# Kernel optimization log

Measured on AMD Instinct MI355X. Metric: run time of the kernel, lower is better.

Reference implementation:

```python
import jax, jax.numpy as jnp
import numpy as np

POOL = 7
IMG_H, IMG_W = 1024, 1024
CANONICAL = 224.0  # canonical box size used in the FPN level assignment


def _crop_and_resize(fm, boxes, ph, pw):
    """TF-style crop_and_resize (extrapolation_value=0).

    fm: [C, H, W] feature map; boxes: [N, 4] normalized (y1, x1, y2, x2).
    Returns [N, C, ph, pw] bilinearly sampled crops.
    """
    C, H, W = fm.shape
    y1, x1, y2, x2 = boxes[:, 0], boxes[:, 1], boxes[:, 2], boxes[:, 3]
    ty = jnp.arange(ph, dtype=boxes.dtype) / (ph - 1)  # [ph] in [0,1]
    tx = jnp.arange(pw, dtype=boxes.dtype) / (pw - 1)
    ys = (y1[:, None] + (y2 - y1)[:, None] * ty) * (H - 1)  # [N, ph] image coords
    xs = (x1[:, None] + (x2 - x1)[:, None] * tx) * (W - 1)  # [N, pw]
    yy = jnp.broadcast_to(ys[:, :, None], (ys.shape[0], ph, pw))  # [N, ph, pw]
    xx = jnp.broadcast_to(xs[:, None, :], (xs.shape[0], ph, pw))
    y0f = jnp.floor(yy)
    x0f = jnp.floor(xx)
    wy = yy - y0f
    wx = xx - x0f
    y0 = jnp.clip(y0f.astype(jnp.int32), 0, H - 1)
    y1i = jnp.clip(y0 + 1, 0, H - 1)
    x0 = jnp.clip(x0f.astype(jnp.int32), 0, W - 1)
    x1i = jnp.clip(x0 + 1, 0, W - 1)

    def g(yi, xi):
        return fm[:, yi, xi]  # [C, N, ph, pw]

    val = (g(y0, x0) * ((1 - wy) * (1 - wx))[None]
           + g(y0, x1i) * ((1 - wy) * wx)[None]
           + g(y1i, x0) * (wy * (1 - wx))[None]
           + g(y1i, x1i) * (wy * wx)[None])
    # extrapolation_value = 0 for samples outside the feature map
    inb = (yy >= 0) & (yy <= H - 1) & (xx >= 0) & (xx <= W - 1)
    val = jnp.where(inb[None], val, 0.0)
    return jnp.transpose(val, (1, 0, 2, 3))  # [N, C, ph, pw]


def setup_inputs() -> dict:
    key = jax.random.key(0)
    k1, k2, k3, k4, k5, k6, k7, k8 = jax.random.split(key, 8)
    N = 1000
    y1 = jax.random.uniform(k1, (N, 1)) * 0.7
    x1 = jax.random.uniform(k2, (N, 1)) * 0.7
    hh = jax.random.uniform(k3, (N, 1)) * 0.28 + 0.02
    ww = jax.random.uniform(k4, (N, 1)) * 0.28 + 0.02
    boxes = jnp.concatenate([y1, x1, y1 + hh, x1 + ww], axis=1)[None]  # [1,N,4]
    C = 256
    p2 = jax.random.normal(k5, (1, C, 256, 256), dtype=jnp.float32)
    p3 = jax.random.normal(k6, (1, C, 128, 128), dtype=jnp.float32)
    p4 = jax.random.normal(k7, (1, C, 64, 64), dtype=jnp.float32)
    p5 = jax.random.normal(k8, (1, C, 32, 32), dtype=jnp.float32)
    return {"boxes": boxes, "p2": p2, "p3": p3, "p4": p4, "p5": p5}


def reference(boxes, p2, p3, p4, p5):
    boxes = boxes[0]  # squeeze batch, [N,4]
    fms = [p2[0], p3[0], p4[0], p5[0]]  # each [C,H,W]
    y1, x1, y2, x2 = boxes[:, 0:1], boxes[:, 1:2], boxes[:, 2:3], boxes[:, 3:4]
    h = y2 - y1
    w = x2 - x1
    image_area = jnp.asarray(float(IMG_H * IMG_W), dtype=boxes.dtype)
    roi_level = 4 + jnp.log2(jnp.sqrt(h * w) / (CANONICAL / jnp.sqrt(image_area)))
    roi_level = jnp.clip(jnp.round(roi_level), 2, 5).astype(jnp.int32)[:, 0]  # [N]
    # Boxes are detached before cropping in the original (level_boxes.detach()).
    crop_boxes = jax.lax.stop_gradient(boxes)
    out = jnp.zeros((boxes.shape[0], fms[0].shape[0], POOL, POOL), dtype=boxes.dtype)
    for i, level in enumerate(range(2, 6)):
        crop = _crop_and_resize(fms[i], crop_boxes, POOL, POOL)
        sel = (roi_level == level)[:, None, None, None]
        out = out + jnp.where(sel, crop, 0.0)
    return out  # [N, C, POOL, POOL], original box order (sort restores order)
```

## Files before the change

kernel.cpp:

```cpp
#include <hip/hip_runtime.h>

#define POOL 7
#define NCH 256
#define OUT_PER_BOX (NCH * POOL * POOL)
#define PARTS 7
#define PART_SZ (OUT_PER_BOX / PARTS)
#define ITERS (PART_SZ / 256)

__global__ __launch_bounds__(256) void roi_align_kernel(
    const float* __restrict__ boxes,
    const float* __restrict__ p2,
    const float* __restrict__ p3,
    const float* __restrict__ p4,
    const float* __restrict__ p5,
    float* __restrict__ out,
    int nbox)
{
    const int n    = blockIdx.x % nbox;
    const int part = blockIdx.x / nbox;
    const int tid  = threadIdx.x;

    __shared__ int   s_y0[POOL], s_y1[POOL], s_xb[POOL], s_xcl[POOL];
    __shared__ float s_wy[POOL], s_wx[POOL], s_vy[POOL], s_vx[POOL];

    const float by1 = boxes[n * 4 + 0];
    const float bx1 = boxes[n * 4 + 1];
    const float by2 = boxes[n * 4 + 2];
    const float bx2 = boxes[n * 4 + 3];
    const float h = by2 - by1;
    const float w = bx2 - bx1;

    const float lvlf = 4.0f + log2f(sqrtf(h * w) / 0.21875f);
    int lvl = (int)rintf(lvlf);
    lvl = lvl < 2 ? 2 : (lvl > 5 ? 5 : lvl);

    const float* fm;
    int H;
    switch (lvl) {
        case 2:  fm = p2; H = 256; break;
        case 3:  fm = p3; H = 128; break;
        case 4:  fm = p4; H = 64;  break;
        default: fm = p5; H = 32;  break;
    }
    const float Hm1 = (float)(H - 1);

    if (tid < POOL) {
        const float t = (float)tid * (1.0f / 6.0f);

        const float yy  = (by1 + h * t) * Hm1;
        const float y0f = floorf(yy);
        int y0 = (int)y0f;
        y0 = min(H - 1, max(0, y0));
        s_y0[tid] = y0;
        s_y1[tid] = min(H - 1, y0 + 1);
        s_wy[tid] = yy - y0f;
        s_vy[tid] = (yy >= 0.0f && yy <= Hm1) ? 1.0f : 0.0f;

        const float xx  = (bx1 + w * t) * Hm1;
        const float x0f = floorf(xx);
        int x0 = (int)x0f;
        x0 = min(H - 1, max(0, x0));
        s_xb[tid]  = min(x0, H - 2);
        s_xcl[tid] = (x0 == H - 1) ? 1 : 0;
        s_wx[tid]  = xx - x0f;
        s_vx[tid]  = (xx >= 0.0f && xx <= Hm1) ? 1.0f : 0.0f;
    }
    __syncthreads();

    const size_t out_base = (size_t)n * OUT_PER_BOX + (size_t)part * PART_SZ;
    const int idx0 = part * PART_SZ + tid;
    const int HW = H * H;

    float2 q0[ITERS], q1[ITERS];
    #pragma unroll
    for (int i = 0; i < ITERS; ++i) {
        const int idx = idx0 + i * 256;
        const int c  = idx / 49;
        const int r  = idx - c * 49;
        const int py = r / 7;
        const int px = r - py * 7;

        const float* fmc = fm + (size_t)c * HW;
        const int xb = s_xb[px];
        q0[i] = *(const float2*)(fmc + s_y0[py] * H + xb);
        q1[i] = *(const float2*)(fmc + s_y1[py] * H + xb);
    }

    #pragma unroll
    for (int i = 0; i < ITERS; ++i) {
        const int idx = idx0 + i * 256;
        const int c  = idx / 49;
        const int r  = idx - c * 49;
        const int py = r / 7;
        const int px = r - py * 7;

        const float wy = s_wy[py], wx = s_wx[px];
        const int   cl = s_xcl[px];

        const float v00 = cl ? q0[i].y : q0[i].x;
        const float v01 = q0[i].y;
        const float v10 = cl ? q1[i].y : q1[i].x;
        const float v11 = q1[i].y;

        const float r0 = v00 + wx * (v01 - v00);
        const float r1 = v10 + wx * (v11 - v10);
        float val = (r0 + wy * (r1 - r0)) * s_vy[py] * s_vx[px];

        out[out_base + (size_t)(i * 256 + tid)] = val;
    }
}

extern "C" void kernel_launch(void* const* d_in, const int* in_sizes, int n_in,
                              void* d_out, int out_size, void* d_ws, size_t ws_size,
                              hipStream_t stream) {
    const float* boxes = (const float*)d_in[0];
    const float* p2    = (const float*)d_in[1];
    const float* p3    = (const float*)d_in[2];
    const float* p4    = (const float*)d_in[3];
    const float* p5    = (const float*)d_in[4];
    float* out         = (float*)d_out;

    const int nbox = in_sizes[0] / 4;
    roi_align_kernel<<<nbox * PARTS, 256, 0, stream>>>(boxes, p2, p3, p4, p5, out, nbox);
}
```

Baseline: 155.0 us.

## Stage ROI feature regions in LDS per channel group, gather fallback for large boxes

Adds a staged kernel where each block handles one box and 16 channels. It copies the box's bounding feature-map window into shared memory with row-contiguous loads, using magic-number division for the indexing, then does the bilinear interpolation from LDS. Boxes whose window does not fit the LDS buffer are handled by the original scattered-gather kernel, launched second; each of its blocks exits early when its box was already staged. This trades the scattered float2 global gathers for more, but coalesced, loads. The cost is a second launch, a 30KB LDS footprint that limits occupancy, and extra bytes read when a window is much larger than the sampled points.

Measured after the change: 203.0 us. 31.0% more time.

```diff
diff --git a/kernel.cpp b/kernel.cpp
--- a/kernel.cpp
+++ b/kernel.cpp
@@ -6,70 +6,183 @@
 #define PARTS 7
 #define PART_SZ (OUT_PER_BOX / PARTS)
 #define ITERS (PART_SZ / 256)
-
-__global__ __launch_bounds__(256) void roi_align_kernel(
+#define CPB 16
+#define NGRP (NCH / CPB)
+#define LDSF 7680
+
+struct Geom {
+    const float* fm;
+    float by1, bx1, h, w, Hm1;
+    int H, ymin, R, xmin, W, Wp;
+};
+
+__device__ __forceinline__ Geom box_geom(
+    const float* __restrict__ boxes, int n,
+    const float* p2, const float* p3, const float* p4, const float* p5)
+{
+    Geom g;
+    g.by1 = boxes[n * 4 + 0];
+    g.bx1 = boxes[n * 4 + 1];
+    const float by2 = boxes[n * 4 + 2];
+    const float bx2 = boxes[n * 4 + 3];
+    g.h = by2 - g.by1;
+    g.w = bx2 - g.bx1;
+    const float lvlf = 4.0f + log2f(sqrtf(g.h * g.w) / 0.21875f);
+    int lvl = (int)rintf(lvlf);
+    lvl = lvl < 2 ? 2 : (lvl > 5 ? 5 : lvl);
+    switch (lvl) {
+        case 2:  g.fm = p2; g.H = 256; break;
+        case 3:  g.fm = p3; g.H = 128; break;
+        case 4:  g.fm = p4; g.H = 64;  break;
+        default: g.fm = p5; g.H = 32;  break;
+    }
+    g.Hm1 = (float)(g.H - 1);
+    int ya = (int)floorf((g.by1 + g.h * 0.0f) * g.Hm1); ya = min(g.H - 1, max(0, ya));
+    int yb = (int)floorf((g.by1 + g.h * 1.0f) * g.Hm1); yb = min(g.H - 1, max(0, yb));
+    int xa = (int)floorf((g.bx1 + g.w * 0.0f) * g.Hm1); xa = min(g.H - 1, max(0, xa));
+    int xc = (int)floorf((g.bx1 + g.w * 1.0f) * g.Hm1); xc = min(g.H - 1, max(0, xc));
+    const int xba = min(xa, g.H - 2);
+    const int xbb = min(xc, g.H - 2);
+    g.ymin = ya;
+    g.R    = min(g.H - 1, yb + 1) - ya + 1;
+    g.xmin = xba;
+    g.W    = xbb + 2 - xba;
+    g.Wp   = g.W | 1;
+    return g;
+}
+
+__device__ __forceinline__ unsigned magic_of(int d) {
+    return (unsigned)((0x100000000ULL + (unsigned)d - 1) / (unsigned)d);
+}
+__device__ __forceinline__ unsigned magic_div(unsigned q, unsigned m) {
+    return (unsigned)(((unsigned long long)q * m) >> 32);
+}
+
+__global__ __launch_bounds__(256) void staged_kernel(
     const float* __restrict__ boxes,
-    const float* __restrict__ p2,
-    const float* __restrict__ p3,
-    const float* __restrict__ p4,
-    const float* __restrict__ p5,
-    float* __restrict__ out,
-    int nbox)
+    const float* __restrict__ p2, const float* __restrict__ p3,
+    const float* __restrict__ p4, const float* __restrict__ p5,
+    float* __restrict__ out, int nbox)
 {
-    const int n    = blockIdx.x % nbox;
-    const int part = blockIdx.x / nbox;
-    const int tid  = threadIdx.x;
-
+    __shared__ float reg[LDSF];
     __shared__ int   s_y0[POOL], s_y1[POOL], s_xb[POOL], s_xcl[POOL];
     __shared__ float s_wy[POOL], s_wx[POOL], s_vy[POOL], s_vx[POOL];
 
-    const float by1 = boxes[n * 4 + 0];
-    const float bx1 = boxes[n * 4 + 1];
-    const float by2 = boxes[n * 4 + 2];
-    const float bx2 = boxes[n * 4 + 3];
-    const float h = by2 - by1;
-    const float w = bx2 - bx1;
-
-    const float lvlf = 4.0f + log2f(sqrtf(h * w) / 0.21875f);
-    int lvl = (int)rintf(lvlf);
-    lvl = lvl < 2 ? 2 : (lvl > 5 ? 5 : lvl);
-
-    const float* fm;
-    int H;
-    switch (lvl) {
-        case 2:  fm = p2; H = 256; break;
-        case 3:  fm = p3; H = 128; break;
-        case 4:  fm = p4; H = 64;  break;
-        default: fm = p5; H = 32;  break;
-    }
-    const float Hm1 = (float)(H - 1);
+    const int bid = blockIdx.x;
+    const int n   = bid / NGRP;
+    const int gr  = bid - n * NGRP;
+    const Geom g = box_geom(boxes, n, p2, p3, p4, p5);
+    if (CPB * g.R * g.Wp > LDSF) return;
+
+    const int tid = threadIdx.x;
+    const int H = g.H, HW = g.H * g.H;
+    const float Hm1 = g.Hm1;
 
     if (tid < POOL) {
-        const float t = (float)tid * (1.0f / 6.0f);
-
-        const float yy  = (by1 + h * t) * Hm1;
+        const float t7 = (float)tid * (1.0f / 6.0f);
+        const float yy  = (g.by1 + g.h * t7) * Hm1;
         const float y0f = floorf(yy);
-        int y0 = (int)y0f;
-        y0 = min(H - 1, max(0, y0));
+        int y0 = (int)y0f; y0 = min(H - 1, max(0, y0));
         s_y0[tid] = y0;
         s_y1[tid] = min(H - 1, y0 + 1);
         s_wy[tid] = yy - y0f;
         s_vy[tid] = (yy >= 0.0f && yy <= Hm1) ? 1.0f : 0.0f;
 
-        const float xx  = (bx1 + w * t) * Hm1;
+        const float xx  = (g.bx1 + g.w * t7) * Hm1;
         const float x0f = floorf(xx);
-        int x0 = (int)x0f;
-        x0 = min(H - 1, max(0, x0));
+        int x0 = (int)x0f; x0 = min(H - 1, max(0, x0));
         s_xb[tid]  = min(x0, H - 2);
         s_xcl[tid] = (x0 == H - 1) ? 1 : 0;
         s_wx[tid]  = xx - x0f;
         s_vx[tid]  = (xx >= 0.0f && xx <= Hm1) ? 1.0f : 0.0f;
     }
+
+    const int c0  = gr * CPB;
+    const int RW  = g.R * g.W;
+    const int tot = CPB * RW;
+    const unsigned mRW = magic_of(RW);
+    const unsigned mW  = magic_of(g.W);
+    const float* fmbase = g.fm + (size_t)c0 * HW + g.ymin * H + g.xmin;
+    for (int q = tid; q < tot; q += 256) {
+        const int ch  = (int)magic_div((unsigned)q, mRW);
+        const int rem = q - ch * RW;
+        const int r   = (int)magic_div((unsigned)rem, mW);
+        const int col = rem - r * g.W;
+        reg[ch * (g.R * g.Wp) + r * g.Wp + col] =
+            fmbase[(size_t)ch * HW + r * H + col];
+    }
+    __syncthreads();
+
+    const size_t ob = (size_t)n * OUT_PER_BOX + (size_t)c0 * 49;
+    #pragma unroll
+    for (int i0 = 0; i0 < CPB * 49; i0 += 256) {
+        const int i = i0 + tid;
+        if (i < CPB * 49) {
+            const int cl  = i / 49;
+            const int pos = i - cl * 49;
+            const int py  = pos / 7;
+            const int px  = pos - py * 7;
+
+            const float* base = &reg[cl * (g.R * g.Wp)];
+            const int r0  = s_y0[py] - g.ymin;
+            const int r1  = s_y1[py] - g.ymin;
+            const int xo  = s_xb[px] - g.xmin;
+            const int clx = s_xcl[px];
+
+            const float v00 = base[r0 * g.Wp + xo + clx];
+            const float v01 = base[r0 * g.Wp + xo + 1];
+            const float v10 = base[r1 * g.Wp + xo + clx];
+            const float v11 = base[r1 * g.Wp + xo + 1];
+
+            const float wy = s_wy[py], wx = s_wx[px];
+            const float a0 = v00 + wx * (v01 - v00);
+            const float a1 = v10 + wx * (v11 - v10);
+            out[ob + i] = (a0 + wy * (a1 - a0)) * s_vy[py] * s_vx[px];
+        }
+    }
+}
+
+__global__ __launch_bounds__(256) void gather_kernel(
+    const float* __restrict__ boxes,
+    const float* __restrict__ p2, const float* __restrict__ p3,
+    const float* __restrict__ p4, const float* __restrict__ p5,
+    float* __restrict__ out, int nbox)
+{
+    const int n    = blockIdx.x % nbox;
+    const int part = blockIdx.x / nbox;
+    const Geom g = box_geom(boxes, n, p2, p3, p4, p5);
+    if (CPB * g.R * g.Wp <= LDSF) return;
+
+    __shared__ int   s_y0[POOL], s_y1[POOL], s_xb[POOL], s_xcl[POOL];
+    __shared__ float s_wy[POOL], s_wx[POOL], s_vy[POOL], s_vx[POOL];
+
+    const int tid = threadIdx.x;
+    const int H = g.H, HW = g.H * g.H;
+    const float Hm1 = g.Hm1;
+    const float* fm = g.fm;
+
+    if (tid < POOL) {
+        const float t7 = (float)tid * (1.0f / 6.0f);
+        const float yy  = (g.by1 + g.h * t7) * Hm1;
+        const float y0f = floorf(yy);
+        int y0 = (int)y0f; y0 = min(H - 1, max(0, y0));
+        s_y0[tid] = y0;
+        s_y1[tid] = min(H - 1, y0 + 1);
+        s_wy[tid] = yy - y0f;
+        s_vy[tid] = (yy >= 0.0f && yy <= Hm1) ? 1.0f : 0.0f;
+
+        const float xx  = (g.bx1 + g.w * t7) * Hm1;
+        const float x0f = floorf(xx);
+        int x0 = (int)x0f; x0 = min(H - 1, max(0, x0));
+        s_xb[tid]  = min(x0, H - 2);
+        s_xcl[tid] = (x0 == H - 1) ? 1 : 0;
+        s_wx[tid]  = xx - x0f;
+        s_vx[tid]  = (xx >= 0.0f && xx <= Hm1) ? 1.0f : 0.0f;
+    }
     __syncthreads();
 
     const size_t out_base = (size_t)n * OUT_PER_BOX + (size_t)part * PART_SZ;
     const int idx0 = part * PART_SZ + tid;
-    const int HW = H * H;
 
     float2 q0[ITERS], q1[ITERS];
     #pragma unroll
@@ -79,13 +192,11 @@
         const int r  = idx - c * 49;
         const int py = r / 7;
         const int px = r - py * 7;
-
         const float* fmc = fm + (size_t)c * HW;
         const int xb = s_xb[px];
         q0[i] = *(const float2*)(fmc + s_y0[py] * H + xb);
         q1[i] = *(const float2*)(fmc + s_y1[py] * H + xb);
     }
-
     #pragma unroll
     for (int i = 0; i < ITERS; ++i) {
         const int idx = idx0 + i * 256;
@@ -93,20 +204,16 @@
         const int r  = idx - c * 49;
         const int py = r / 7;
         const int px = r - py * 7;
-
         const float wy = s_wy[py], wx = s_wx[px];
         const int   cl = s_xcl[px];
-
         const float v00 = cl ? q0[i].y : q0[i].x;
         const float v01 = q0[i].y;
         const float v10 = cl ? q1[i].y : q1[i].x;
         const float v11 = q1[i].y;
-
         const float r0 = v00 + wx * (v01 - v00);
         const float r1 = v10 + wx * (v11 - v10);
-        float val = (r0 + wy * (r1 - r0)) * s_vy[py] * s_vx[px];
-
-        out[out_base + (size_t)(i * 256 + tid)] = val;
+        out[out_base + (size_t)(i * 256 + tid)] =
+            (r0 + wy * (r1 - r0)) * s_vy[py] * s_vx[px];
     }
 }
 
@@ -121,5 +228,9 @@
     float* out         = (float*)d_out;
 
     const int nbox = in_sizes[0] / 4;
-    roi_align_kernel<<<nbox * PARTS, 256, 0, stream>>>(boxes, p2, p3, p4, p5, out, nbox);
-}
+
+    staged_kernel<<<nbox * NGRP, 256, 0, stream>>>(
+        boxes, p2, p3, p4, p5, out, nbox);
+    gather_kernel<<<nbox * PARTS, 256, 0, stream>>>(
+        boxes, p2, p3, p4, p5, out, nbox);
+}
```

## Transpose coarse FPN levels to HWC and gather channel-contiguous bilinear samples

Applied to the files above, without the earlier changes.

Adds a pre-pass that transposes the p3–p5 feature maps from CHW into an HWC workspace. Boxes on those levels are then sampled by a new kernel that reads channel-contiguous float2 pairs and stages results in shared memory for coalesced output writes. Level-2 boxes keep the original CHW gather in their own kernel. This targets the uncoalesced per-channel strided gathers, at the cost of rereading and rewriting about 22 MB of feature maps on every call plus two extra kernel launches.

Measured after the change: 162.7 us. 4.9% more time.

```diff
diff --git a/kernel.cpp b/kernel.cpp
--- a/kernel.cpp
+++ b/kernel.cpp
@@ -7,21 +7,51 @@
 #define PART_SZ (OUT_PER_BOX / PARTS)
 #define ITERS (PART_SZ / 256)
 
-__global__ __launch_bounds__(256) void roi_align_kernel(
+#define HW3 16384
+#define HW4 4096
+#define HW5 1024
+#define T3_FLOATS (HW3 * NCH)
+#define T4_FLOATS (HW4 * NCH)
+#define T5_FLOATS (HW5 * NCH)
+#define TILES3 (HW3 / 64 * 4)
+#define TILES4 (HW4 / 64 * 4)
+#define TILES5 (HW5 / 64 * 4)
+#define NTILES (TILES3 + TILES4 + TILES5)
+
+__global__ __launch_bounds__(256) void transpose_kernel(
+    const float* __restrict__ p3, const float* __restrict__ p4,
+    const float* __restrict__ p5, float* __restrict__ T3,
+    float* __restrict__ T4, float* __restrict__ T5)
+{
+    __shared__ float tile[64][65];
+    int bid = blockIdx.x;
+    const float* src; float* dst; int HW;
+    if (bid < TILES3)                { src = p3; dst = T3; HW = HW3; }
+    else if (bid < TILES3 + TILES4)  { bid -= TILES3; src = p4; dst = T4; HW = HW4; }
+    else                             { bid -= TILES3 + TILES4; src = p5; dst = T5; HW = HW5; }
+
+    const int ct  = bid & 3;
+    const int hwt = bid >> 2;
+    const int c0  = ct * 64, hw0 = hwt * 64;
+    const int tx  = threadIdx.x & 63, ty = threadIdx.x >> 6;
+
+    #pragma unroll
+    for (int r = ty; r < 64; r += 4)
+        tile[r][tx] = src[(size_t)(c0 + r) * HW + hw0 + tx];
+    __syncthreads();
+    #pragma unroll
+    for (int r = ty; r < 64; r += 4)
+        dst[(size_t)(hw0 + r) * 256 + c0 + tx] = tile[tx][r];
+}
+
+__global__ __launch_bounds__(256) void hwc_kernel(
     const float* __restrict__ boxes,
-    const float* __restrict__ p2,
-    const float* __restrict__ p3,
-    const float* __restrict__ p4,
-    const float* __restrict__ p5,
-    float* __restrict__ out,
-    int nbox)
+    const float* __restrict__ T3, const float* __restrict__ T4,
+    const float* __restrict__ T5, float* __restrict__ out, int nbox)
 {
-    const int n    = blockIdx.x % nbox;
-    const int part = blockIdx.x / nbox;
-    const int tid  = threadIdx.x;
-
-    __shared__ int   s_y0[POOL], s_y1[POOL], s_xb[POOL], s_xcl[POOL];
-    __shared__ float s_wy[POOL], s_wx[POOL], s_vy[POOL], s_vx[POOL];
+    const int n  = blockIdx.x >> 1;
+    const int hb = blockIdx.x & 1;
+    if (n >= nbox) return;
 
     const float by1 = boxes[n * 4 + 0];
     const float bx1 = boxes[n * 4 + 1];
@@ -29,7 +59,196 @@
     const float bx2 = boxes[n * 4 + 3];
     const float h = by2 - by1;
     const float w = bx2 - bx1;
-
+    const float lvlf = 4.0f + log2f(sqrtf(h * w) / 0.21875f);
+    int lvl = (int)rintf(lvlf);
+    lvl = lvl < 2 ? 2 : (lvl > 5 ? 5 : lvl);
+    if (lvl == 2) return;
+
+    const float* T; int H;
+    if (lvl == 3)      { T = T3; H = 128; }
+    else if (lvl == 4) { T = T4; H = 64;  }
+    else               { T = T5; H = 32;  }
+    const float Hm1 = (float)(H - 1);
+
+    __shared__ float obuf[49][132];
+    __shared__ int   s_y0[POOL], s_y1[POOL], s_xb[POOL], s_xcl[POOL];
+    __shared__ float s_wy[POOL], s_wx[POOL], s_vy[POOL], s_vx[POOL];
+
+    const int tid = threadIdx.x;
+    if (tid < POOL) {
+        const float t7 = (float)tid * (1.0f / 6.0f);
+
+        const float yy  = (by1 + h * t7) * Hm1;
+        const float y0f = floorf(yy);
+        int y0 = (int)y0f; y0 = min(H - 1, max(0, y0));
+        s_y0[tid] = y0;
+        s_y1[tid] = min(H - 1, y0 + 1);
+        s_wy[tid] = yy - y0f;
+        s_vy[tid] = (yy >= 0.0f && yy <= Hm1) ? 1.0f : 0.0f;
+
+        const float xx  = (bx1 + w * t7) * Hm1;
+        const float x0f = floorf(xx);
+        int x0 = (int)x0f; x0 = min(H - 1, max(0, x0));
+        s_xb[tid]  = min(x0, H - 2);
+        s_xcl[tid] = (x0 == H - 1) ? 1 : 0;
+        s_wx[tid]  = xx - x0f;
+        s_vx[tid]  = (xx >= 0.0f && xx <= Hm1) ? 1.0f : 0.0f;
+    }
+    __syncthreads();
+
+    const int wv = tid >> 6;
+    const int ln = tid & 63;
+    const int cb = hb * 128 + 2 * ln;
+
+    for (int pos = wv; pos < 49; pos += 4) {
+        const int py = pos / 7;
+        const int px = pos - py * 7;
+        const int y0 = s_y0[py], y1 = s_y1[py];
+        const int xb = s_xb[px], cl = s_xcl[px];
+
+        const size_t a0 = ((size_t)(y0 * H + xb) << 8) + cb;
+        const size_t a1 = ((size_t)(y1 * H + xb) << 8) + cb;
+        const float2 A0 = *(const float2*)&T[a0];
+        const float2 A1 = *(const float2*)&T[a0 + 256];
+        const float2 B0 = *(const float2*)&T[a1];
+        const float2 B1 = *(const float2*)&T[a1 + 256];
+
+        const float wy = s_wy[py], wx = s_wx[px];
+        const float vv = s_vy[py] * s_vx[px];
+
+        float2 o;
+        {
+            const float v00 = cl ? A1.x : A0.x;
+            const float v01 = A1.x;
+            const float v10 = cl ? B1.x : B0.x;
+            const float v11 = B1.x;
+            const float r0 = v00 + wx * (v01 - v00);
+            const float r1 = v10 + wx * (v11 - v10);
+            o.x = (r0 + wy * (r1 - r0)) * vv;
+        }
+        {
+            const float v00 = cl ? A1.y : A0.y;
+            const float v01 = A1.y;
+            const float v10 = cl ? B1.y : B0.y;
+            const float v11 = B1.y;
+            const float r0 = v00 + wx * (v01 - v00);
+            const float r1 = v10 + wx * (v11 - v10);
+            o.y = (r0 + wy * (r1 - r0)) * vv;
+        }
+        *(float2*)&obuf[pos][2 * ln] = o;
+    }
+    __syncthreads();
+
+    const size_t ob = (size_t)n * OUT_PER_BOX + (size_t)hb * 128 * 49;
+    for (int i = tid; i < 128 * 49; i += 256) {
+        const int c   = i / 49;
+        const int pos = i - c * 49;
+        out[ob + i] = obuf[pos][c];
+    }
+}
+
+__global__ __launch_bounds__(256) void gather2_kernel(
+    const float* __restrict__ boxes,
+    const float* __restrict__ p2,
+    float* __restrict__ out, int nbox)
+{
+    const int n    = blockIdx.x % nbox;
+    const int part = blockIdx.x / nbox;
+    const int tid  = threadIdx.x;
+
+    const float by1 = boxes[n * 4 + 0];
+    const float bx1 = boxes[n * 4 + 1];
+    const float by2 = boxes[n * 4 + 2];
+    const float bx2 = boxes[n * 4 + 3];
+    const float h = by2 - by1;
+    const float w = bx2 - bx1;
+    const float lvlf = 4.0f + log2f(sqrtf(h * w) / 0.21875f);
+    int lvl = (int)rintf(lvlf);
+    lvl = lvl < 2 ? 2 : (lvl > 5 ? 5 : lvl);
+    if (lvl != 2) return;
+
+    const float* fm = p2;
+    const int H = 256;
+    const int HW = 65536;
+    const float Hm1 = 255.0f;
+
+    __shared__ int   s_y0[POOL], s_y1[POOL], s_xb[POOL], s_xcl[POOL];
+    __shared__ float s_wy[POOL], s_wx[POOL], s_vy[POOL], s_vx[POOL];
+
+    if (tid < POOL) {
+        const float t7 = (float)tid * (1.0f / 6.0f);
+        const float yy  = (by1 + h * t7) * Hm1;
+        const float y0f = floorf(yy);
+        int y0 = (int)y0f; y0 = min(H - 1, max(0, y0));
+        s_y0[tid] = y0;
+        s_y1[tid] = min(H - 1, y0 + 1);
+        s_wy[tid] = yy - y0f;
+        s_vy[tid] = (yy >= 0.0f && yy <= Hm1) ? 1.0f : 0.0f;
+        const float xx  = (bx1 + w * t7) * Hm1;
+        const float x0f = floorf(xx);
+        int x0 = (int)x0f; x0 = min(H - 1, max(0, x0));
+        s_xb[tid]  = min(x0, H - 2);
+        s_xcl[tid] = (x0 == H - 1) ? 1 : 0;
+        s_wx[tid]  = xx - x0f;
+        s_vx[tid]  = (xx >= 0.0f && xx <= Hm1) ? 1.0f : 0.0f;
+    }
+    __syncthreads();
+
+    const size_t out_base = (size_t)n * OUT_PER_BOX + (size_t)part * PART_SZ;
+    const int idx0 = part * PART_SZ + tid;
+
+    float2 q0[ITERS], q1[ITERS];
+    #pragma unroll
+    for (int i = 0; i < ITERS; ++i) {
+        const int idx = idx0 + i * 256;
+        const int c  = idx / 49;
+        const int r  = idx - c * 49;
+        const int py = r / 7;
+        const int px = r - py * 7;
+        const float* fmc = fm + (size_t)c * HW;
+        const int xb = s_xb[px];
+        q0[i] = *(const float2*)(fmc + s_y0[py] * H + xb);
+        q1[i] = *(const float2*)(fmc + s_y1[py] * H + xb);
+    }
+    #pragma unroll
+    for (int i = 0; i < ITERS; ++i) {
+        const int idx = idx0 + i * 256;
+        const int c  = idx / 49;
+        const int r  = idx - c * 49;
+        const int py = r / 7;
+        const int px = r - py * 7;
+        const float wy = s_wy[py], wx = s_wx[px];
+        const int   cl = s_xcl[px];
+        const float v00 = cl ? q0[i].y : q0[i].x;
+        const float v01 = q0[i].y;
+        const float v10 = cl ? q1[i].y : q1[i].x;
+        const float v11 = q1[i].y;
+        const float r0 = v00 + wx * (v01 - v00);
+        const float r1 = v10 + wx * (v11 - v10);
+        out[out_base + (size_t)(i * 256 + tid)] =
+            (r0 + wy * (r1 - r0)) * s_vy[py] * s_vx[px];
+    }
+}
+
+__global__ __launch_bounds__(256) void roi_align_flat_kernel(
+    const float* __restrict__ boxes,
+    const float* __restrict__ p2, const float* __restrict__ p3,
+    const float* __restrict__ p4, const float* __restrict__ p5,
+    float* __restrict__ out, int nbox)
+{
+    const int n    = blockIdx.x % nbox;
+    const int part = blockIdx.x / nbox;
+    const int tid  = threadIdx.x;
+
+    __shared__ int   s_y0[POOL], s_y1[POOL], s_xb[POOL], s_xcl[POOL];
+    __shared__ float s_wy[POOL], s_wx[POOL], s_vy[POOL], s_vx[POOL];
+
+    const float by1 = boxes[n * 4 + 0];
+    const float bx1 = boxes[n * 4 + 1];
+    const float by2 = boxes[n * 4 + 2];
+    const float bx2 = boxes[n * 4 + 3];
+    const float h = by2 - by1;
+    const float w = bx2 - bx1;
     const float lvlf = 4.0f + log2f(sqrtf(h * w) / 0.21875f);
     int lvl = (int)rintf(lvlf);
     lvl = lvl < 2 ? 2 : (lvl > 5 ? 5 : lvl);
@@ -45,21 +264,17 @@
     const float Hm1 = (float)(H - 1);
 
     if (tid < POOL) {
-        const float t = (float)tid * (1.0f / 6.0f);
-
-        const float yy  = (by1 + h * t) * Hm1;
+        const float t7 = (float)tid * (1.0f / 6.0f);
+        const float yy  = (by1 + h * t7) * Hm1;
         const float y0f = floorf(yy);
-        int y0 = (int)y0f;
-        y0 = min(H - 1, max(0, y0));
+        int y0 = (int)y0f; y0 = min(H - 1, max(0, y0));
         s_y0[tid] = y0;
         s_y1[tid] = min(H - 1, y0 + 1);
         s_wy[tid] = yy - y0f;
         s_vy[tid] = (yy >= 0.0f && yy <= Hm1) ? 1.0f : 0.0f;
-
-        const float xx  = (bx1 + w * t) * Hm1;
+        const float xx  = (bx1 + w * t7) * Hm1;
         const float x0f = floorf(xx);
-        int x0 = (int)x0f;
-        x0 = min(H - 1, max(0, x0));
+        int x0 = (int)x0f; x0 = min(H - 1, max(0, x0));
         s_xb[tid]  = min(x0, H - 2);
         s_xcl[tid] = (x0 == H - 1) ? 1 : 0;
         s_wx[tid]  = xx - x0f;
@@ -79,13 +294,11 @@
         const int r  = idx - c * 49;
         const int py = r / 7;
         const int px = r - py * 7;
-
         const float* fmc = fm + (size_t)c * HW;
         const int xb = s_xb[px];
         q0[i] = *(const float2*)(fmc + s_y0[py] * H + xb);
         q1[i] = *(const float2*)(fmc + s_y1[py] * H + xb);
     }
-
     #pragma unroll
     for (int i = 0; i < ITERS; ++i) {
         const int idx = idx0 + i * 256;
@@ -93,20 +306,16 @@
         const int r  = idx - c * 49;
         const int py = r / 7;
         const int px = r - py * 7;
-
         const float wy = s_wy[py], wx = s_wx[px];
         const int   cl = s_xcl[px];
-
         const float v00 = cl ? q0[i].y : q0[i].x;
         const float v01 = q0[i].y;
         const float v10 = cl ? q1[i].y : q1[i].x;
         const float v11 = q1[i].y;
-
         const float r0 = v00 + wx * (v01 - v00);
         const float r1 = v10 + wx * (v11 - v10);
-        float val = (r0 + wy * (r1 - r0)) * s_vy[py] * s_vx[px];
-
-        out[out_base + (size_t)(i * 256 + tid)] = val;
+        out[out_base + (size_t)(i * 256 + tid)] =
+            (r0 + wy * (r1 - r0)) * s_vy[py] * s_vx[px];
     }
 }
 
@@ -121,5 +330,19 @@
     float* out         = (float*)d_out;
 
     const int nbox = in_sizes[0] / 4;
-    roi_align_kernel<<<nbox * PARTS, 256, 0, stream>>>(boxes, p2, p3, p4, p5, out, nbox);
-}
+    const size_t need = (size_t)(T3_FLOATS + T4_FLOATS + T5_FLOATS) * sizeof(float);
+
+    if (ws_size < need) {
+        roi_align_flat_kernel<<<nbox * PARTS, 256, 0, stream>>>(
+            boxes, p2, p3, p4, p5, out, nbox);
+        return;
+    }
+
+    float* T3 = (float*)d_ws;
+    float* T4 = T3 + T3_FLOATS;
+    float* T5 = T4 + T4_FLOATS;
+
+    transpose_kernel<<<NTILES, 256, 0, stream>>>(p3, p4, p5, T3, T4, T5);
+    hwc_kernel<<<2 * nbox, 256, 0, stream>>>(boxes, T3, T4, T5, out, nbox);
+    gather2_kernel<<<nbox * PARTS, 256, 0, stream>>>(boxes, p2, out, nbox);
+}
```
